# Performance work log

Hardware: AMD Instinct MI355X
Metric: run time of the kernel (lower is better)

## Reference

```python
import jax, jax.numpy as jnp
import numpy as np

N_NODES = 100000
N_GRAPHS = 64
NEG_SLOPE = 0.1


def lrelu(x):
    return jnp.where(x > 0, x, NEG_SLOPE * x)


def gcn_layer(x, W, b, src, dst, deg_inv_sqrt):
    # PyG GCNConv: x' = D^-1/2 (A + I) D^-1/2 (x W) + b
    h = x @ W  # [N, out]
    norm = (deg_inv_sqrt[src] * deg_inv_sqrt[dst])[:, None]  # [E, 1]
    agg = jax.ops.segment_sum(h[src] * norm, dst, num_segments=N_NODES)
    agg = agg + h * (deg_inv_sqrt ** 2)[:, None]  # self-loop contribution
    return agg + b


def setup_inputs() -> dict:
    key = jax.random.key(0)
    ks = jax.random.split(key, 12)
    E = 1600000
    x = jax.random.normal(ks[0], (N_NODES, 128), dtype=jnp.float32)
    edge_index = jax.random.randint(ks[1], (2, E), 0, N_NODES, dtype=jnp.int32)
    batch = jnp.sort(jax.random.randint(ks[2], (N_NODES,), 0, N_GRAPHS, dtype=jnp.int32))

    def glorot(k, shape):
        fan_in, fan_out = shape
        s = jnp.sqrt(6.0 / (fan_in + fan_out))
        return jax.random.uniform(k, shape, jnp.float32, -s, s)

    return {
        "x": x,
        "edge_index": edge_index,
        "batch": batch,
        "W1": glorot(ks[3], (128, 32)),
        "b1": jnp.zeros((32,), jnp.float32),
        "W2": glorot(ks[4], (32, 64)),
        "b2": jnp.zeros((64,), jnp.float32),
        "Wl1": glorot(ks[5], (64, 128)),
        "bl1": jnp.zeros((128,), jnp.float32),
        "Wl2": glorot(ks[6], (128, 64)),
        "bl2": jnp.zeros((64,), jnp.float32),
        "Wl3": glorot(ks[7], (64, 1)),
        "bl3": jnp.zeros((1,), jnp.float32),
    }


def reference(x, edge_index, batch, W1, b1, W2, b2, Wl1, bl1, Wl2, bl2, Wl3, bl3):
    src, dst = edge_index[0], edge_index[1]
    # degree with self-loops (symmetric norm, all edge weights = 1)
    deg = jax.ops.segment_sum(jnp.ones_like(src, dtype=x.dtype), dst, num_segments=N_NODES) + 1.0
    deg_inv_sqrt = jax.lax.rsqrt(deg)

    h = lrelu(gcn_layer(x, W1, b1, src, dst, deg_inv_sqrt))
    h = gcn_layer(h, W2, b2, src, dst, deg_inv_sqrt)
    g = jax.ops.segment_max(h, batch, num_segments=N_GRAPHS)  # global max pool [G, 64]
    g = lrelu(g @ Wl1 + bl1)
    g = lrelu(g @ Wl2 + bl2)
    return g @ Wl3 + bl3  # [G, 1]
```

## Files before the change

### kernel.cpp

```cpp
#include <hip/hip_runtime.h>
#include <hip/hip_fp16.h>
#include <math.h>

#define N_NODES 100000
#define N_EDGES 1600000
#define N_GRAPHS 64
#define NB 391
#define CAP 5504

__device__ __forceinline__ unsigned f2o(float f) {
    unsigned u = __float_as_uint(f);
    return (u & 0x80000000u) ? ~u : (u | 0x80000000u);
}
__device__ __forceinline__ float o2f(unsigned u) {
    return (u & 0x80000000u) ? __uint_as_float(u & 0x7fffffffu) : __uint_as_float(~u);
}

__device__ __forceinline__ float4 cvt8(float2 raw) {
    __half2 h0 = ((const __half2*)&raw)[0];
    __half2 h1 = ((const __half2*)&raw)[1];
    float2 f0 = __half22float2(h0);
    float2 f1 = __half22float2(h1);
    return make_float4(f0.x, f0.y, f1.x, f1.y);
}
__device__ __forceinline__ float4 loadh8(const __half* p) {
    return cvt8(*(const float2*)p);
}
__device__ __forceinline__ void storeh8(__half* p, float4 v) {
    __half2 o0 = __floats2half2_rn(v.x, v.y);
    __half2 o1 = __floats2half2_rn(v.z, v.w);
    float2 ow;
    ((__half2*)&ow)[0] = o0;
    ((__half2*)&ow)[1] = o1;
    *(float2*)p = ow;
}

__global__ __launch_bounds__(256) void bucket_kernel(const int* __restrict__ src, const int* __restrict__ dst,
                                                     int* __restrict__ bucketCursor, unsigned* __restrict__ ebuf) {
    __shared__ int hist[NB];
    __shared__ int cur[NB];
    int tid = threadIdx.x;
    for (int b = tid; b < NB; b += 256) hist[b] = 0;
    __syncthreads();
    int e0 = blockIdx.x * 3200;
    for (int i = tid; i < 3200; i += 256) {
        int d = dst[e0 + i];
        atomicAdd(&hist[d >> 8], 1);
    }
    __syncthreads();
    for (int b = tid; b < NB; b += 256) {
        int h = hist[b];
        cur[b] = h ? atomicAdd(&bucketCursor[b], h) : 0;
    }
    __syncthreads();
    for (int i = tid; i < 3200; i += 256) {
        int d = dst[e0 + i];
        int s = src[e0 + i];
        int bu = d >> 8;
        int pos = atomicAdd(&cur[bu], 1);
        if (pos < CAP)
            ebuf[(size_t)bu * CAP + pos] = ((unsigned)(d & 255) << 24) | (unsigned)s;
    }
}

__global__ __launch_bounds__(256) void csr_kernel(const unsigned* __restrict__ ebuf,
                                                  const int* __restrict__ bucketCursor,
                                                  int* __restrict__ colb, int* __restrict__ rowptr,
                                                  int* __restrict__ cnt, float* __restrict__ dis) {
    __shared__ unsigned stage[CAP];
    __shared__ int c256[256], row256[256], cur256[256];
    int b = blockIdx.x;
    int tid = threadIdx.x;
    int M = bucketCursor[b];
    if (M > CAP) M = CAP;
    c256[tid] = 0;
    __syncthreads();
    const unsigned* eb = ebuf + (size_t)b * CAP;
    for (int i = tid; i < M; i += 256) atomicAdd(&c256[eb[i] >> 24], 1);
    __syncthreads();
    if (tid < 64) {
        int c0 = c256[tid * 4], c1 = c256[tid * 4 + 1], c2 = c256[tid * 4 + 2], c3 = c256[tid * 4 + 3];
        int s = c0 + c1 + c2 + c3;
        int inc = s;
        #pragma unroll
        for (int o = 1; o < 64; o <<= 1) {
            int v = __shfl_up(inc, o, 64);
            if (tid >= o) inc += v;
        }
        int ex = inc - s;
        row256[tid * 4] = ex;
        row256[tid * 4 + 1] = ex + c0;
        row256[tid * 4 + 2] = ex + c0 + c1;
        row256[tid * 4 + 3] = ex + c0 + c1 + c2;
    }
    __syncthreads();
    cur256[tid] = row256[tid];
    int node = (b << 8) + tid;
    if (node < N_NODES) {
        int c = c256[tid];
        cnt[node] = c;
        dis[node] = rsqrtf((float)(c + 1));
        rowptr[node] = b * CAP + row256[tid];
    }
    __syncthreads();
    for (int i = tid; i < M; i += 256) {
        unsigned p = eb[i];
        int slot = atomicAdd(&cur256[p >> 24], 1);
        stage[slot] = p & 0xFFFFFFu;
    }
    __syncthreads();
    for (int i = tid; i < M; i += 256) colb[b * CAP + i] = (int)stage[i];
}

__global__ __launch_bounds__(256) void gemm1_kernel(const float* __restrict__ x, const float* __restrict__ W1,
                                                    const float* __restrict__ dis, __half* __restrict__ hs1h) {
    __shared__ float xs[64][128];
    __shared__ float wt[32][132];
    int tid = threadIdx.x;
    int r0 = blockIdx.x * 64;
    for (int idx = tid; idx < 128 * 32; idx += 256) {
        int k = idx >> 5, j = idx & 31;
        wt[j][k] = W1[idx];
    }
    for (int idx = tid; idx < 64 * 32; idx += 256) {
        int r = idx >> 5, kc = idx & 31;
        int gr = r0 + r;
        float4 v = (gr < N_NODES) ? ((const float4*)x)[(size_t)gr * 32 + kc] : make_float4(0.f, 0.f, 0.f, 0.f);
        *(float4*)&xs[r][kc * 4] = v;
    }
    __syncthreads();
    int j = tid & 31;
    int rr = tid >> 5;
    float acc[8];
    #pragma unroll
    for (int i = 0; i < 8; i++) acc[i] = 0.f;
    for (int kc = 0; kc < 128; kc += 4) {
        float4 wv = *(const float4*)&wt[j][kc];
        #pragma unroll
        for (int i = 0; i < 8; i++) {
            float4 xv = *(const float4*)&xs[rr + i * 8][kc];
            acc[i] += xv.x * wv.x + xv.y * wv.y + xv.z * wv.z + xv.w * wv.w;
        }
    }
    #pragma unroll
    for (int i = 0; i < 8; i++) {
        int gr = r0 + rr + i * 8;
        if (gr < N_NODES) hs1h[(size_t)gr * 32 + j] = __float2half_rn(dis[gr] * acc[i]);
    }
}

__global__ __launch_bounds__(256) void agg1_kernel(const __half* __restrict__ hs1h, const int* __restrict__ colb,
                                                   const int* __restrict__ rowptr, const int* __restrict__ cnt,
                                                   const float* __restrict__ dis, const float* __restrict__ b1,
                                                   __half* __restrict__ t1h) {
    const int ROWS = 8;
    int tid = threadIdx.x;
    int wid = tid >> 6;
    int lane = tid & 63;
    int es = lane >> 3;
    int q = lane & 7;
    int w = blockIdx.x * 4 + wid;
    int r0 = w * ROWS;

    const float2 z2 = make_float2(0.f, 0.f);
    int st = rowptr[r0];
    int n = cnt[r0];
    float2 pS = z2, p0 = z2, p1 = z2, p2 = z2, p3 = z2;
    if (es == 0) pS = *(const float2*)(hs1h + (size_t)r0 * 32 + q * 4);
    {
        int e0 = es, e1 = 8 + es, e2 = 16 + es, e3 = 24 + es;
        if (e0 < n) p0 = *(const float2*)(hs1h + (size_t)colb[st + e0] * 32 + q * 4);
        if (e1 < n) p1 = *(const float2*)(hs1h + (size_t)colb[st + e1] * 32 + q * 4);
        if (e2 < n) p2 = *(const float2*)(hs1h + (size_t)colb[st + e2] * 32 + q * 4);
        if (e3 < n) p3 = *(const float2*)(hs1h + (size_t)colb[st + e3] * 32 + q * 4);
    }
    for (int i = 0; i < ROWS; i++) {
        int r = r0 + i;
        int stA = st, nA = n;
        float2 rS = pS, r0v = p0, r1v = p1, r2v = p2, r3v = p3;
        pS = z2; p0 = z2; p1 = z2; p2 = z2; p3 = z2;
        if (i + 1 < ROWS) {
            int rn = r + 1;
            st = rowptr[rn];
            n = cnt[rn];
            if (es == 0) pS = *(const float2*)(hs1h + (size_t)rn * 32 + q * 4);
            int e0 = es, e1 = 8 + es, e2 = 16 + es, e3 = 24 + es;
            if (e0 < n) p0 = *(const float2*)(hs1h + (size_t)colb[st + e0] * 32 + q * 4);
            if (e1 < n) p1 = *(const float2*)(hs1h + (size_t)colb[st + e1] * 32 + q * 4);
            if (e2 < n) p2 = *(const float2*)(hs1h + (size_t)colb[st + e2] * 32 + q * 4);
            if (e3 < n) p3 = *(const float2*)(hs1h + (size_t)colb[st + e3] * 32 + q * 4);
        }
        float4 s = cvt8(rS), a0 = cvt8(r0v), a1 = cvt8(r1v), a2 = cvt8(r2v), a3 = cvt8(r3v);
        float4 a;
        a.x = (s.x + (a0.x + a1.x)) + (a2.x + a3.x);
        a.y = (s.y + (a0.y + a1.y)) + (a2.y + a3.y);
        a.z = (s.z + (a0.z + a1.z)) + (a2.z + a3.z);
        a.w = (s.w + (a0.w + a1.w)) + (a2.w + a3.w);
        for (int k = 32; k < nA; k += 16) {
            int e0 = k + es, e1 = k + 8 + es;
            if (e0 < nA) {
                float4 v = loadh8(hs1h + (size_t)colb[stA + e0] * 32 + q * 4);
                a.x += v.x; a.y += v.y; a.z += v.z; a.w += v.w;
            }
            if (e1 < nA) {
                float4 v = loadh8(hs1h + (size_t)colb[stA + e1] * 32 + q * 4);
                a.x += v.x; a.y += v.y; a.z += v.z; a.w += v.w;
            }
        }
        #pragma unroll
        for (int m = 8; m < 64; m <<= 1) {
            a.x += __shfl_xor(a.x, m, 64);
            a.y += __shfl_xor(a.y, m, 64);
            a.z += __shfl_xor(a.z, m, 64);
            a.w += __shfl_xor(a.w, m, 64);
        }
        if (es == 0) {
            float4 bv = *(const float4*)&b1[q * 4];
            float dr = dis[r];
            float4 v;
            v.x = dr * a.x + bv.x; v.y = dr * a.y + bv.y; v.z = dr * a.z + bv.z; v.w = dr * a.w + bv.w;
            v.x = v.x > 0.f ? v.x : 0.1f * v.x;
            v.y = v.y > 0.f ? v.y : 0.1f * v.y;
            v.z = v.z > 0.f ? v.z : 0.1f * v.z;
            v.w = v.w > 0.f ? v.w : 0.1f * v.w;
            v.x *= dr; v.y *= dr; v.z *= dr; v.w *= dr;
            storeh8(t1h + (size_t)r * 32 + q * 4, v);
        }
    }
}

__global__ __launch_bounds__(256) void agg2_kernel(const __half* __restrict__ t1h, const int* __restrict__ colb,
                                                   const int* __restrict__ rowptr, const int* __restrict__ cnt,
                                                   const float* __restrict__ dis,
                                                   float* __restrict__ agg32) {
    const int ROWS = 8;
    int tid = threadIdx.x;
    int wid = tid >> 6;
    int lane = tid & 63;
    int es = lane >> 3;
    int q = lane & 7;
    int w = blockIdx.x * 4 + wid;
    int r0 = w * ROWS;

    const float2 z2 = make_float2(0.f, 0.f);
    int st = rowptr[r0];
    int n = cnt[r0];
    float2 pS = z2, p0 = z2, p1 = z2, p2 = z2, p3 = z2;
    if (es == 0) pS = *(const float2*)(t1h + (size_t)r0 * 32 + q * 4);
    {
        int e0 = es, e1 = 8 + es, e2 = 16 + es, e3 = 24 + es;
        if (e0 < n) p0 = *(const float2*)(t1h + (size_t)colb[st + e0] * 32 + q * 4);
        if (e1 < n) p1 = *(const float2*)(t1h + (size_t)colb[st + e1] * 32 + q * 4);
        if (e2 < n) p2 = *(const float2*)(t1h + (size_t)colb[st + e2] * 32 + q * 4);
        if (e3 < n) p3 = *(const float2*)(t1h + (size_t)colb[st + e3] * 32 + q * 4);
    }
    for (int i = 0; i < ROWS; i++) {
        int r = r0 + i;
        int stA = st, nA = n;
        float2 rS = pS, r0v = p0, r1v = p1, r2v = p2, r3v = p3;
        pS = z2; p0 = z2; p1 = z2; p2 = z2; p3 = z2;
        if (i + 1 < ROWS) {
            int rn = r + 1;
            st = rowptr[rn];
            n = cnt[rn];
            if (es == 0) pS = *(const float2*)(t1h + (size_t)rn * 32 + q * 4);
            int e0 = es, e1 = 8 + es, e2 = 16 + es, e3 = 24 + es;
            if (e0 < n) p0 = *(const float2*)(t1h + (size_t)colb[st + e0] * 32 + q * 4);
            if (e1 < n) p1 = *(const float2*)(t1h + (size_t)colb[st + e1] * 32 + q * 4);
            if (e2 < n) p2 = *(const float2*)(t1h + (size_t)colb[st + e2] * 32 + q * 4);
            if (e3 < n) p3 = *(const float2*)(t1h + (size_t)colb[st + e3] * 32 + q * 4);
        }
        float4 s = cvt8(rS), a0 = cvt8(r0v), a1 = cvt8(r1v), a2 = cvt8(r2v), a3 = cvt8(r3v);
        float4 a;
        a.x = (s.x + (a0.x + a1.x)) + (a2.x + a3.x);
        a.y = (s.y + (a0.y + a1.y)) + (a2.y + a3.y);
        a.z = (s.z + (a0.z + a1.z)) + (a2.z + a3.z);
        a.w = (s.w + (a0.w + a1.w)) + (a2.w + a3.w);
        for (int k = 32; k < nA; k += 16) {
            int e0 = k + es, e1 = k + 8 + es;
            if (e0 < nA) {
                float4 v = loadh8(t1h + (size_t)colb[stA + e0] * 32 + q * 4);
                a.x += v.x; a.y += v.y; a.z += v.z; a.w += v.w;
            }
            if (e1 < nA) {
                float4 v = loadh8(t1h + (size_t)colb[stA + e1] * 32 + q * 4);
                a.x += v.x; a.y += v.y; a.z += v.z; a.w += v.w;
            }
        }
        #pragma unroll
        for (int m = 8; m < 64; m <<= 1) {
            a.x += __shfl_xor(a.x, m, 64);
            a.y += __shfl_xor(a.y, m, 64);
            a.z += __shfl_xor(a.z, m, 64);
            a.w += __shfl_xor(a.w, m, 64);
        }
        if (es == 0) {
            float dr = dis[r];
            float4 o = make_float4(dr * a.x, dr * a.y, dr * a.z, dr * a.w);
            *(float4*)&agg32[(size_t)r * 32 + q * 4] = o;
        }
    }
}

__global__ __launch_bounds__(256) void gemm2p_kernel(const float* __restrict__ agg32, const float* __restrict__ W2,
                                                     const float* __restrict__ b2, const int* __restrict__ batch,
                                                     unsigned* __restrict__ gbufu) {
    __shared__ float as1[64][32];
    __shared__ float w2s[32][64];
    __shared__ float red[4][64];
    int tid = threadIdx.x;
    int r0 = blockIdx.x * 64;
    for (int idx = tid; idx < 32 * 64; idx += 256) w2s[idx >> 6][idx & 63] = W2[idx];
    for (int idx = tid; idx < 64 * 8; idx += 256) {
        int rl = idx >> 3, qc = idx & 7;
        int gr = r0 + rl;
        float4 v = (gr < N_NODES) ? ((const float4*)agg32)[(size_t)gr * 8 + qc] : make_float4(0.f, 0.f, 0.f, 0.f);
        *(float4*)&as1[rl][qc * 4] = v;
    }
    __syncthreads();
    int j = tid & 63;
    int rq = tid >> 6;
    float w2c[32];
    #pragma unroll
    for (int k = 0; k < 32; k++) w2c[k] = w2s[k][j];
    float bj = b2[j];
    int rend = (r0 + 64 <= N_NODES) ? 64 : (N_NODES - r0);
    int gfirst = batch[r0];
    int glast = batch[r0 + rend - 1];
    bool uni = (gfirst == glast);
    float runmax = -INFINITY;
    for (int i = 0; i < 16; i++) {
        int rl = rq + i * 4;
        if (rl >= rend) break;
        float acc = bj;
        #pragma unroll
        for (int kc = 0; kc < 32; kc += 4) {
            float4 av = *(const float4*)&as1[rl][kc];
            acc += av.x * w2c[kc] + av.y * w2c[kc + 1] + av.z * w2c[kc + 2] + av.w * w2c[kc + 3];
        }
        if (uni) runmax = fmaxf(runmax, acc);
        else atomicMax(&gbufu[batch[r0 + rl] * 64 + j], f2o(acc));
    }
    if (uni) {
        red[rq][j] = runmax;
        __syncthreads();
        if (tid < 64) {
            float m = fmaxf(fmaxf(red[0][tid], red[1][tid]), fmaxf(red[2][tid], red[3][tid]));
            atomicMax(&gbufu[gfirst * 64 + tid], f2o(m));
        }
    }
}

__global__ __launch_bounds__(256) void mlp_kernel(const unsigned* __restrict__ gbufu,
                                                  const float* __restrict__ Wl1, const float* __restrict__ bl1,
                                                  const float* __restrict__ Wl2, const float* __restrict__ bl2,
                                                  const float* __restrict__ Wl3, const float* __restrict__ bl3,
                                                  float* __restrict__ out) {
    __shared__ float A[64][64];
    __shared__ float B[64][128];
    int tid = threadIdx.x;
    for (int idx = tid; idx < 64 * 64; idx += 256) A[idx >> 6][idx & 63] = o2f(gbufu[idx]);
    __syncthreads();
    {
        int j = tid & 127;
        int rg = tid >> 7;
        float wc[64];
        #pragma unroll
        for (int k = 0; k < 64; k++) wc[k] = Wl1[k * 128 + j];
        float bj = bl1[j];
        for (int r = rg; r < 64; r += 2) {
            float acc = bj;
            #pragma unroll
            for (int kc = 0; kc < 64; kc += 4) {
                float4 av = *(const float4*)&A[r][kc];
                acc += av.x * wc[kc] + av.y * wc[kc + 1] + av.z * wc[kc + 2] + av.w * wc[kc + 3];
            }
            B[r][j] = acc > 0.f ? acc : 0.1f * acc;
        }
    }
    __syncthreads();
    {
        int j = tid & 63;
        int rg = tid >> 6;
        float wc[128];
        #pragma unroll
        for (int k = 0; k < 128; k++) wc[k] = Wl2[k * 64 + j];
        float bj = bl2[j];
        for (int r = rg; r < 64; r += 4) {
            float acc = bj;
            #pragma unroll
            for (int kc = 0; kc < 128; kc += 4) {
                float4 bv = *(const float4*)&B[r][kc];
                acc += bv.x * wc[kc] + bv.y * wc[kc + 1] + bv.z * wc[kc + 2] + bv.w * wc[kc + 3];
            }
            A[r][j] = acc > 0.f ? acc : 0.1f * acc;
        }
    }
    __syncthreads();
    if (tid < 64) {
        int r = tid;
        float acc = bl3[0];
        #pragma unroll
        for (int k = 0; k < 64; k++) acc += A[r][k] * Wl3[k];
        out[r] = acc;
    }
}

extern "C" void kernel_launch(void* const* d_in, const int* in_sizes, int n_in,
                              void* d_out, int out_size, void* d_ws, size_t ws_size,
                              hipStream_t stream) {
    (void)in_sizes; (void)n_in; (void)out_size; (void)ws_size;
    const float* x    = (const float*)d_in[0];
    const int*   edge = (const int*)d_in[1];
    const int*   batch= (const int*)d_in[2];
    const float* W1   = (const float*)d_in[3];
    const float* b1   = (const float*)d_in[4];
    const float* W2   = (const float*)d_in[5];
    const float* b2   = (const float*)d_in[6];
    const float* Wl1  = (const float*)d_in[7];
    const float* bl1  = (const float*)d_in[8];
    const float* Wl2  = (const float*)d_in[9];
    const float* bl2  = (const float*)d_in[10];
    const float* Wl3  = (const float*)d_in[11];
    const float* bl3  = (const float*)d_in[12];
    const int* srcp = edge;
    const int* dstp = edge + N_EDGES;

    char* ws = (char*)d_ws;
    int*      bucketCursor = (int*)ws;
    unsigned* gbufu        = (unsigned*)(bucketCursor + NB);
    size_t zeroed = (size_t)(NB + N_GRAPHS * 64) * 4;
    size_t off = (zeroed + 255) & ~(size_t)255;
    auto alloc = [&](size_t bytes) { char* p = ws + off; off = (off + bytes + 255) & ~(size_t)255; return p; };
    float*    dis    = (float*)alloc((size_t)N_NODES * 4);
    int*      cnt    = (int*)alloc((size_t)N_NODES * 4);
    int*      rowptr = (int*)alloc((size_t)N_NODES * 4);
    unsigned* ebuf   = (unsigned*)alloc((size_t)NB * CAP * 4);
    int*      colb   = (int*)alloc((size_t)NB * CAP * 4);
    __half*   hs1h   = (__half*)alloc((size_t)N_NODES * 32 * 2);
    __half*   t1h    = (__half*)alloc((size_t)N_NODES * 32 * 2);
    float*    agg32  = (float*)alloc((size_t)N_NODES * 32 * 4);

    hipMemsetAsync(ws, 0, zeroed, stream);

    bucket_kernel<<<500, 256, 0, stream>>>(srcp, dstp, bucketCursor, ebuf);
    csr_kernel   <<<NB, 256, 0, stream>>>(ebuf, bucketCursor, colb, rowptr, cnt, dis);
    gemm1_kernel <<<(N_NODES + 63) / 64, 256, 0, stream>>>(x, W1, dis, hs1h);
    agg1_kernel  <<<3125, 256, 0, stream>>>(hs1h, colb, rowptr, cnt, dis, b1, t1h);
    agg2_kernel  <<<3125, 256, 0, stream>>>(t1h, colb, rowptr, cnt, dis, agg32);
    gemm2p_kernel<<<(N_NODES + 63) / 64, 256, 0, stream>>>(agg32, W2, b2, batch, gbufu);
    mlp_kernel   <<<1, 256, 0, stream>>>(gbufu, Wl1, bl1, Wl2, bl2, Wl3, bl3, (float*)d_out);
}
```

Baseline: 299.7 us.

## Rewrite gemm1 with fp16 shared tiles, 4x4 register blocking and fdot2

Measured after the change: 298.9 us. No clear change (-0.3%).

```diff
diff --git a/kernel.cpp b/kernel.cpp
--- a/kernel.cpp
+++ b/kernel.cpp
@@ -35,6 +35,9 @@
     *(float2*)p = ow;
 }
 
+typedef _Float16 h2r __attribute__((ext_vector_type(2)));
+union HB { float4 f4; h2r h[4]; };
+
 __global__ __launch_bounds__(256) void bucket_kernel(const int* __restrict__ src, const int* __restrict__ dst,
                                                      int* __restrict__ bucketCursor, unsigned* __restrict__ ebuf) {
     __shared__ int hist[NB];
@@ -114,38 +117,62 @@
 
 __global__ __launch_bounds__(256) void gemm1_kernel(const float* __restrict__ x, const float* __restrict__ W1,
                                                     const float* __restrict__ dis, __half* __restrict__ hs1h) {
-    __shared__ float xs[64][128];
-    __shared__ float wt[32][132];
-    int tid = threadIdx.x;
-    int r0 = blockIdx.x * 64;
+    __shared__ __half xsh[128][136];
+    __shared__ __half wth[32][136];
+    int tid = threadIdx.x;
+    int r0 = blockIdx.x * 128;
     for (int idx = tid; idx < 128 * 32; idx += 256) {
         int k = idx >> 5, j = idx & 31;
-        wt[j][k] = W1[idx];
-    }
-    for (int idx = tid; idx < 64 * 32; idx += 256) {
-        int r = idx >> 5, kc = idx & 31;
+        wth[j][k] = __float2half_rn(W1[idx]);
+    }
+    for (int idx = tid; idx < 128 * 32; idx += 256) {
+        int r = idx >> 5, c4 = idx & 31;
         int gr = r0 + r;
-        float4 v = (gr < N_NODES) ? ((const float4*)x)[(size_t)gr * 32 + kc] : make_float4(0.f, 0.f, 0.f, 0.f);
-        *(float4*)&xs[r][kc * 4] = v;
-    }
-    __syncthreads();
-    int j = tid & 31;
-    int rr = tid >> 5;
-    float acc[8];
+        float4 v = (gr < N_NODES) ? ((const float4*)x)[(size_t)gr * 32 + c4] : make_float4(0.f, 0.f, 0.f, 0.f);
+        __half* p = &xsh[r][c4 * 4];
+        *(__half2*)p       = __floats2half2_rn(v.x, v.y);
+        *(__half2*)(p + 2) = __floats2half2_rn(v.z, v.w);
+    }
+    __syncthreads();
+    int jg = tid & 7;
+    int rg = tid >> 3;
+    float acc[4][4];
     #pragma unroll
-    for (int i = 0; i < 8; i++) acc[i] = 0.f;
-    for (int kc = 0; kc < 128; kc += 4) {
-        float4 wv = *(const float4*)&wt[j][kc];
-        #pragma unroll
-        for (int i = 0; i < 8; i++) {
-            float4 xv = *(const float4*)&xs[rr + i * 8][kc];
-            acc[i] += xv.x * wv.x + xv.y * wv.y + xv.z * wv.z + xv.w * wv.w;
+    for (int i = 0; i < 4; i++)
+        #pragma unroll
+        for (int j = 0; j < 4; j++) acc[i][j] = 0.f;
+    for (int kc = 0; kc < 128; kc += 8) {
+        HB xr[4], wr[4];
+        #pragma unroll
+        for (int ri = 0; ri < 4; ri++) xr[ri].f4 = *(const float4*)&xsh[rg + 32 * ri][kc];
+        #pragma unroll
+        for (int jj = 0; jj < 4; jj++) wr[jj].f4 = *(const float4*)&wth[jg * 4 + jj][kc];
+        #pragma unroll
+        for (int ri = 0; ri < 4; ri++) {
+            #pragma unroll
+            for (int jj = 0; jj < 4; jj++) {
+                #pragma unroll
+                for (int t = 0; t < 4; t++) {
+#if defined(__has_builtin) && __has_builtin(__builtin_amdgcn_fdot2)
+                    acc[ri][jj] = __builtin_amdgcn_fdot2(xr[ri].h[t], wr[jj].h[t], acc[ri][jj], false);
+#else
+                    acc[ri][jj] += (float)xr[ri].h[t][0] * (float)wr[jj].h[t][0]
+                                 + (float)xr[ri].h[t][1] * (float)wr[jj].h[t][1];
+#endif
+                }
+            }
         }
     }
     #pragma unroll
-    for (int i = 0; i < 8; i++) {
-        int gr = r0 + rr + i * 8;
-        if (gr < N_NODES) hs1h[(size_t)gr * 32 + j] = __float2half_rn(dis[gr] * acc[i]);
+    for (int ri = 0; ri < 4; ri++) {
+        int gr = r0 + rg + 32 * ri;
+        if (gr < N_NODES) {
+            float dr = dis[gr];
+            float2 ow;
+            ((__half2*)&ow)[0] = __floats2half2_rn(dr * acc[ri][0], dr * acc[ri][1]);
+            ((__half2*)&ow)[1] = __floats2half2_rn(dr * acc[ri][2], dr * acc[ri][3]);
+            *(float2*)&hs1h[(size_t)gr * 32 + jg * 4] = ow;
+        }
     }
 }
 
@@ -445,7 +472,7 @@
 
     bucket_kernel<<<500, 256, 0, stream>>>(srcp, dstp, bucketCursor, ebuf);
     csr_kernel   <<<NB, 256, 0, stream>>>(ebuf, bucketCursor, colb, rowptr, cnt, dis);
-    gemm1_kernel <<<(N_NODES + 63) / 64, 256, 0, stream>>>(x, W1, dis, hs1h);
+    gemm1_kernel <<<(N_NODES + 127) / 128, 256, 0, stream>>>(x, W1, dis, hs1h);
     agg1_kernel  <<<3125, 256, 0, stream>>>(hs1h, colb, rowptr, cnt, dis, b1, t1h);
     agg2_kernel  <<<3125, 256, 0, stream>>>(t1h, colb, rowptr, cnt, dis, agg32);
     gemm2p_kernel<<<(N_NODES + 63) / 64, 256, 0, stream>>>(agg32, W2, b2, batch, gbufu);
```
